# Optimization experiments

Hardware: AMD Instinct MI355X
Metric: run time of the kernel (lower is better)

The kernel has to match this reference:

```python
import jax, jax.numpy as jnp
import numpy as np

B, S_ENC, S_DEC, ENC_H, DEC_H = 8, 2048, 2048, 512, 512


def setup_inputs() -> dict:
    key = jax.random.key(0)
    k1, k2, k3 = jax.random.split(key, 3)
    return {
        "enc_hidden_states": jax.random.normal(k1, (B, S_ENC, ENC_H), dtype=jnp.float32),
        "dec_hidden_states": jax.random.normal(k2, (B, S_DEC, DEC_H), dtype=jnp.float32),
        "W_att": jax.random.normal(k3, (ENC_H, DEC_H), dtype=jnp.float32),
    }


def reference(enc_hidden_states, dec_hidden_states, W_att):
    # Project encoder states: [B, S_enc, dec_h]
    enc_proj = jnp.einsum("bse,ed->bsd", enc_hidden_states, W_att)
    # Luong 'general' scores for all decoder timesteps at once: [B, S_dec, S_enc]
    # (original code loops over decoder timesteps via tf.map_fn; this is the
    # equivalent single batched matmul)
    att_logits = jnp.einsum("btd,bsd->bts", dec_hidden_states, enc_proj)
    att_softmax = jax.nn.softmax(att_logits, axis=-1)
    # Attention context vectors: [B, S_dec, enc_h]
    att_vector = jnp.einsum("bts,bse->bte", att_softmax, enc_hidden_states)
    return att_vector
```

## Files before the change

kernel.cpp:

```cpp
#include <hip/hip_runtime.h>
#include <cstdint>


#define DEVINL __device__ __forceinline__

typedef __attribute__((ext_vector_type(8))) short short8;
typedef __attribute__((ext_vector_type(4))) float f32x4;

DEVINL short f2bf(float x) {
    union { float f; uint32_t u; } v; v.f = x;
    uint32_t r = v.u + 0x7FFFu + ((v.u >> 16) & 1u);
    return (short)(r >> 16);
}
DEVINL float bf2f(short h) {
    union { uint32_t u; float f; } v; v.u = ((uint32_t)(uint16_t)h) << 16;
    return v.f;
}

DEVINL void gload_lds16(const void* g, void* l) {
    __builtin_amdgcn_global_load_lds(
        (const __attribute__((address_space(1))) char*)g,
        (__attribute__((address_space(3))) char*)l, 16, 0, 0);
}

__global__ __launch_bounds__(256)
void split_kernel(const float* __restrict__ x, short* __restrict__ hi,
                  short* __restrict__ lo)
{
    long i = ((long)blockIdx.x * 256 + threadIdx.x) * 8;
    f32x4 a = *(const f32x4*)(x + i);
    f32x4 b = *(const f32x4*)(x + i + 4);
    short8 h, l;
#pragma unroll
    for (int j = 0; j < 4; j++) {
        short ha = f2bf(a[j]); h[j] = ha;     l[j] = f2bf(a[j] - bf2f(ha));
        short hb = f2bf(b[j]); h[4 + j] = hb; l[4 + j] = f2bf(b[j] - bf2f(hb));
    }
    *(short8*)(hi + i) = h;
    *(short8*)(lo + i) = l;
}

__global__ __launch_bounds__(256)
void split_w_kernel(const float* __restrict__ w, short* __restrict__ wth,
                    short* __restrict__ wtl)
{
    int idx = blockIdx.x * 256 + threadIdx.x;
    int k = idx >> 9, n = idx & 511;
    float v = w[idx];
    short h = f2bf(v);
    wth[(long)n * 512 + k] = h;
    wtl[(long)n * 512 + k] = f2bf(v - bf2f(h));
}

__global__ __launch_bounds__(256)
void transpose_bf16_kernel(const float* __restrict__ x, short* __restrict__ xt)
{
    __shared__ short tile[32][33];
    const int b  = blockIdx.z;
    const int s0 = blockIdx.x * 32;
    const int e0 = blockIdx.y * 32;
    const float* px = x + (long)b * 2048 * 512;
    short* pt = xt + (long)b * 512 * 2048;
    const int tx = threadIdx.x & 31;
    const int ty = threadIdx.x >> 5;
#pragma unroll
    for (int r = 0; r < 32; r += 8)
        tile[ty + r][tx] = f2bf(px[(long)(s0 + ty + r) * 512 + e0 + tx]);
    __syncthreads();
#pragma unroll
    for (int r = 0; r < 32; r += 8)
        pt[(long)(e0 + ty + r) * 2048 + s0 + tx] = tile[tx][ty + r];
}

template<int NTERMS, bool SPLIT_OUT>
__global__ __launch_bounds__(256, 2)
void gemm_bt(const short* __restrict__ Ah, const short* __restrict__ Al,
             const short* __restrict__ Bh, const short* __restrict__ Bl,
             float* __restrict__ C, short* __restrict__ Ch, short* __restrict__ Cl,
             int K, int lda, int ldb, int ldc,
             long sA, long sB, long sC)
{
    extern __shared__ char smem_raw[];
    constexpr int OPS = (NTERMS == 3) ? 4 : 2;
    constexpr int SET = 128 * 32 * OPS;
    short* smem = (short*)smem_raw;

    const int tid  = threadIdx.x;
    const int wave = tid >> 6;
    const int lane = tid & 63;
    const int quad = lane >> 4;
    const int l16  = lane & 15;
    const int wm   = (wave >> 1) * 64;
    const int wn   = (wave & 1) * 64;

    const long tile_m = (long)blockIdx.y * 128;
    const long tile_n = (long)blockIdx.x * 128;
    const int  bz     = blockIdx.z;

    const short* pAh = Ah + (long)bz * sA;
    const short* pBh = Bh + (long)bz * sB;
    const short* pAl = (NTERMS == 3) ? (Al + (long)bz * sA) : nullptr;
    const short* pBl = (NTERMS == 3) ? (Bl + (long)bz * sB) : nullptr;

    const int srow = tid >> 2;
    const int skq  = (tid & 3) * 8;
    const int lds_off = srow * 32 + skq;
    const long ga0 = (tile_m + srow) * (long)lda + skq;
    const long gb0 = (tile_n + srow) * (long)ldb + skq;

    auto stage = [&](int k0, int buf) {
        short* s   = smem + buf * SET;
        short* ash = s;
        short* bsh = s + 128 * 32;
        gload_lds16(pAh + ga0 + k0,             ash + lds_off);
        gload_lds16(pAh + ga0 + 64l * lda + k0, ash + lds_off + 64 * 32);
        gload_lds16(pBh + gb0 + k0,             bsh + lds_off);
        gload_lds16(pBh + gb0 + 64l * ldb + k0, bsh + lds_off + 64 * 32);
        if constexpr (NTERMS == 3) {
            short* asl = s + 2 * 128 * 32;
            short* bsl = s + 3 * 128 * 32;
            gload_lds16(pAl + ga0 + k0,             asl + lds_off);
            gload_lds16(pAl + ga0 + 64l * lda + k0, asl + lds_off + 64 * 32);
            gload_lds16(pBl + gb0 + k0,             bsl + lds_off);
            gload_lds16(pBl + gb0 + 64l * ldb + k0, bsl + lds_off + 64 * 32);
        }
    };

    f32x4 acc[4][4] = {};
    stage(0, 0);
    int cur = 0;

    for (int k0 = 0; k0 < K; k0 += 32) {
        __syncthreads();
        if (k0 + 32 < K) stage(k0 + 32, cur ^ 1);

        short* s   = smem + cur * SET;
        short* ash = s;
        short* bsh = s + 128 * 32;
        short* asl = s + 2 * 128 * 32;
        short* bsl = s + 3 * 128 * 32;

        short8 ah[4], bh[4], al[4], bl[4];
#pragma unroll
        for (int i = 0; i < 4; i++) {
            ah[i] = *(const short8*)&ash[(wm + i * 16 + l16) * 32 + quad * 8];
            bh[i] = *(const short8*)&bsh[(wn + i * 16 + l16) * 32 + quad * 8];
            if constexpr (NTERMS == 3) {
                al[i] = *(const short8*)&asl[(wm + i * 16 + l16) * 32 + quad * 8];
                bl[i] = *(const short8*)&bsl[(wn + i * 16 + l16) * 32 + quad * 8];
            }
        }
#pragma unroll
        for (int i = 0; i < 4; i++)
#pragma unroll
            for (int j = 0; j < 4; j++) {
                acc[i][j] = __builtin_amdgcn_mfma_f32_16x16x32_bf16(ah[i], bh[j], acc[i][j], 0, 0, 0);
                if constexpr (NTERMS == 3) {
                    acc[i][j] = __builtin_amdgcn_mfma_f32_16x16x32_bf16(ah[i], bl[j], acc[i][j], 0, 0, 0);
                    acc[i][j] = __builtin_amdgcn_mfma_f32_16x16x32_bf16(al[i], bh[j], acc[i][j], 0, 0, 0);
                }
            }
        cur ^= 1;
    }

#pragma unroll
    for (int i = 0; i < 4; i++)
#pragma unroll
        for (int j = 0; j < 4; j++) {
            const long row0 = tile_m + wm + i * 16 + quad * 4;
            const long col  = tile_n + wn + j * 16 + l16;
#pragma unroll
            for (int r = 0; r < 4; r++) {
                float v = acc[i][j][r];
                if constexpr (SPLIT_OUT) {
                    long idx = (long)bz * sC + (row0 + r) * (long)ldc + col;
                    short h = f2bf(v);
                    Ch[idx] = h;
                    Cl[idx] = f2bf(v - bf2f(h));
                } else {
                    C[(long)bz * sC + (row0 + r) * (long)ldc + col] = v;
                }
            }
        }
}

__global__ __launch_bounds__(256)
void softmax_kernel(const float* __restrict__ logits, short* __restrict__ P)
{
    const long row = blockIdx.x;
    const float* p = logits + row * 2048;
    const int tid = threadIdx.x;
    const int lane = tid & 63, wave = tid >> 6;

    f32x4 v0 = *(const f32x4*)(p + tid * 8);
    f32x4 v1 = *(const f32x4*)(p + tid * 8 + 4);

    float m = fmaxf(fmaxf(fmaxf(v0[0], v0[1]), fmaxf(v0[2], v0[3])),
                    fmaxf(fmaxf(v1[0], v1[1]), fmaxf(v1[2], v1[3])));
#pragma unroll
    for (int o = 32; o > 0; o >>= 1) m = fmaxf(m, __shfl_xor(m, o));

    __shared__ float red[8];
    if (lane == 0) red[wave] = m;
    __syncthreads();
    m = fmaxf(fmaxf(red[0], red[1]), fmaxf(red[2], red[3]));

    float e[8];
    float s = 0.f;
#pragma unroll
    for (int i = 0; i < 4; i++) { e[i] = __expf(v0[i] - m); s += e[i]; }
#pragma unroll
    for (int i = 0; i < 4; i++) { e[4 + i] = __expf(v1[i] - m); s += e[4 + i]; }
#pragma unroll
    for (int o = 32; o > 0; o >>= 1) s += __shfl_xor(s, o);
    if (lane == 0) red[4 + wave] = s;
    __syncthreads();
    const float inv = 1.f / (red[4] + red[5] + red[6] + red[7]);

    short8 ob;
#pragma unroll
    for (int i = 0; i < 8; i++) ob[i] = f2bf(e[i] * inv);
    *(short8*)(P + row * 2048 + tid * 8) = ob;
}

extern "C" void kernel_launch(void* const* d_in, const int* in_sizes, int n_in,
                              void* d_out, int out_size, void* d_ws, size_t ws_size,
                              hipStream_t stream)
{
    const float* enc = (const float*)d_in[0];
    const float* dec = (const float*)d_in[1];
    const float* W   = (const float*)d_in[2];
    float* out = (float*)d_out;

    const long BSE = 8l * 2048 * 512;
    const long NW  = 512l * 512;

    char* p = (char*)d_ws;
    auto take = [&](long bytes) { char* r = p; p += (bytes + 255) & ~255l; return r; };
    short* enc_hi = (short*)take(BSE * 2);
    short* enc_lo = (short*)take(BSE * 2);
    short* dec_hi = (short*)take(BSE * 2);
    short* dec_lo = (short*)take(BSE * 2);
    short* ep_hi  = (short*)take(BSE * 2);
    short* ep_lo  = (short*)take(BSE * 2);
    short* enc_t  = (short*)take(BSE * 2);
    short* wt_hi  = (short*)take(NW * 2);
    short* wt_lo  = (short*)take(NW * 2);
    float* logits = (float*)take(8l * 2048 * 2048 * 4);
    short* Pbuf = enc_hi;
    (void)ws_size; (void)in_sizes; (void)n_in; (void)out_size;

    split_kernel<<<4096, 256, 0, stream>>>(enc, enc_hi, enc_lo);
    split_kernel<<<4096, 256, 0, stream>>>(dec, dec_hi, dec_lo);
    split_w_kernel<<<1024, 256, 0, stream>>>(W, wt_hi, wt_lo);
    transpose_bf16_kernel<<<dim3(64, 16, 8), 256, 0, stream>>>(enc, enc_t);

    gemm_bt<3, true><<<dim3(4, 128, 1), 256, 64 * 1024, stream>>>(
        enc_hi, enc_lo, wt_hi, wt_lo, nullptr, ep_hi, ep_lo,
        512, 512, 512, 512, 0, 0, 0);

    gemm_bt<3, false><<<dim3(16, 16, 8), 256, 64 * 1024, stream>>>(
        dec_hi, dec_lo, ep_hi, ep_lo, logits, nullptr, nullptr,
        512, 512, 512, 2048, 2048l * 512, 2048l * 512, 2048l * 2048);

    softmax_kernel<<<16384, 256, 0, stream>>>(logits, Pbuf);

    gemm_bt<1, false><<<dim3(4, 16, 8), 256, 32 * 1024, stream>>>(
        Pbuf, nullptr, enc_t, nullptr, out, nullptr, nullptr,
        2048, 2048, 2048, 512, 2048l * 2048, 512l * 2048, 2048l * 512);
}
```

Measured before the change: 355.8 us.

## Fuse softmax into logits GEMM epilogue stats and PV GEMM prologue

The logits GEMM epilogue now computes per-tile row max and exp-sum partials. A small combine kernel merges them into a row max and inverse sum. The P·V GEMM reads fp32 logits directly, applies exp(x - m) while staging its A operand into LDS, and scales by the inverse sum at output. This removes the standalone softmax pass and the bf16 P buffer round trip, and the transpose now reads the existing bf16 hi split instead of fp32. The cost is that the PV kernel reads fp32 logits (twice the bytes of bf16 P) and does the exp inline, and the logits GEMM needs extra LDS and reduction syncs.

```diff
diff --git a/kernel.cpp b/kernel.cpp
--- a/kernel.cpp
+++ b/kernel.cpp
@@ -53,30 +53,31 @@
 }
 
 __global__ __launch_bounds__(256)
-void transpose_bf16_kernel(const float* __restrict__ x, short* __restrict__ xt)
+void transpose_bf16_kernel(const short* __restrict__ x, short* __restrict__ xt)
 {
     __shared__ short tile[32][33];
     const int b  = blockIdx.z;
     const int s0 = blockIdx.x * 32;
     const int e0 = blockIdx.y * 32;
-    const float* px = x + (long)b * 2048 * 512;
+    const short* px = x + (long)b * 2048 * 512;
     short* pt = xt + (long)b * 512 * 2048;
     const int tx = threadIdx.x & 31;
     const int ty = threadIdx.x >> 5;
 #pragma unroll
     for (int r = 0; r < 32; r += 8)
-        tile[ty + r][tx] = f2bf(px[(long)(s0 + ty + r) * 512 + e0 + tx]);
+        tile[ty + r][tx] = px[(long)(s0 + ty + r) * 512 + e0 + tx];
     __syncthreads();
 #pragma unroll
     for (int r = 0; r < 32; r += 8)
         pt[(long)(e0 + ty + r) * 2048 + s0 + tx] = tile[tx][ty + r];
 }
 
-template<int NTERMS, bool SPLIT_OUT>
+template<int NTERMS, bool SPLIT_OUT, bool STATS>
 __global__ __launch_bounds__(256, 2)
 void gemm_bt(const short* __restrict__ Ah, const short* __restrict__ Al,
              const short* __restrict__ Bh, const short* __restrict__ Bl,
              float* __restrict__ C, short* __restrict__ Ch, short* __restrict__ Cl,
+             float2* __restrict__ stats,
              int K, int lda, int ldb, int ldc,
              long sA, long sB, long sC)
 {
@@ -163,6 +164,74 @@
         cur ^= 1;
     }
 
+    if constexpr (STATS) {
+        float* sred = (float*)(smem + 2 * SET);
+        float mrow[4][4], lrow[4][4];
+#pragma unroll
+        for (int i = 0; i < 4; i++)
+#pragma unroll
+            for (int r = 0; r < 4; r++) {
+                float m = acc[i][0][r];
+#pragma unroll
+                for (int j = 1; j < 4; j++) m = fmaxf(m, acc[i][j][r]);
+                m = fmaxf(m, __shfl_xor(m, 1));
+                m = fmaxf(m, __shfl_xor(m, 2));
+                m = fmaxf(m, __shfl_xor(m, 4));
+                m = fmaxf(m, __shfl_xor(m, 8));
+                mrow[i][r] = m;
+            }
+        __syncthreads();
+        if (l16 == 0) {
+#pragma unroll
+            for (int i = 0; i < 4; i++)
+#pragma unroll
+                for (int r = 0; r < 4; r++)
+                    sred[(wm + i * 16 + quad * 4 + r) * 2 + (wave & 1)] = mrow[i][r];
+        }
+        __syncthreads();
+#pragma unroll
+        for (int i = 0; i < 4; i++)
+#pragma unroll
+            for (int r = 0; r < 4; r++) {
+                int row = wm + i * 16 + quad * 4 + r;
+                mrow[i][r] = fmaxf(sred[row * 2], sred[row * 2 + 1]);
+            }
+        __syncthreads();
+#pragma unroll
+        for (int i = 0; i < 4; i++)
+#pragma unroll
+            for (int r = 0; r < 4; r++) {
+                float s = 0.f;
+#pragma unroll
+                for (int j = 0; j < 4; j++) s += __expf(acc[i][j][r] - mrow[i][r]);
+                s += __shfl_xor(s, 1);
+                s += __shfl_xor(s, 2);
+                s += __shfl_xor(s, 4);
+                s += __shfl_xor(s, 8);
+                lrow[i][r] = s;
+            }
+        if (l16 == 0) {
+#pragma unroll
+            for (int i = 0; i < 4; i++)
+#pragma unroll
+                for (int r = 0; r < 4; r++)
+                    sred[(wm + i * 16 + quad * 4 + r) * 2 + (wave & 1)] = lrow[i][r];
+        }
+        __syncthreads();
+        if ((wave & 1) == 0 && l16 == 0) {
+#pragma unroll
+            for (int i = 0; i < 4; i++)
+#pragma unroll
+                for (int r = 0; r < 4; r++) {
+                    int row = wm + i * 16 + quad * 4 + r;
+                    long grow = tile_m + row;
+                    float2 v; v.x = mrow[i][r];
+                    v.y = sred[row * 2] + sred[row * 2 + 1];
+                    stats[((long)bz * 2048 + grow) * 16 + blockIdx.x] = v;
+                }
+        }
+    }
+
 #pragma unroll
     for (int i = 0; i < 4; i++)
 #pragma unroll
@@ -185,42 +254,126 @@
 }
 
 __global__ __launch_bounds__(256)
-void softmax_kernel(const float* __restrict__ logits, short* __restrict__ P)
-{
-    const long row = blockIdx.x;
-    const float* p = logits + row * 2048;
-    const int tid = threadIdx.x;
-    const int lane = tid & 63, wave = tid >> 6;
-
-    f32x4 v0 = *(const f32x4*)(p + tid * 8);
-    f32x4 v1 = *(const f32x4*)(p + tid * 8 + 4);
-
-    float m = fmaxf(fmaxf(fmaxf(v0[0], v0[1]), fmaxf(v0[2], v0[3])),
-                    fmaxf(fmaxf(v1[0], v1[1]), fmaxf(v1[2], v1[3])));
-#pragma unroll
-    for (int o = 32; o > 0; o >>= 1) m = fmaxf(m, __shfl_xor(m, o));
-
-    __shared__ float red[8];
-    if (lane == 0) red[wave] = m;
-    __syncthreads();
-    m = fmaxf(fmaxf(red[0], red[1]), fmaxf(red[2], red[3]));
-
-    float e[8];
-    float s = 0.f;
-#pragma unroll
-    for (int i = 0; i < 4; i++) { e[i] = __expf(v0[i] - m); s += e[i]; }
-#pragma unroll
-    for (int i = 0; i < 4; i++) { e[4 + i] = __expf(v1[i] - m); s += e[4 + i]; }
-#pragma unroll
-    for (int o = 32; o > 0; o >>= 1) s += __shfl_xor(s, o);
-    if (lane == 0) red[4 + wave] = s;
-    __syncthreads();
-    const float inv = 1.f / (red[4] + red[5] + red[6] + red[7]);
-
-    short8 ob;
-#pragma unroll
-    for (int i = 0; i < 8; i++) ob[i] = f2bf(e[i] * inv);
-    *(short8*)(P + row * 2048 + tid * 8) = ob;
+void combine_kernel(const float2* __restrict__ stats, float* __restrict__ Mrow,
+                    float* __restrict__ Linv)
+{
+    long r = (long)blockIdx.x * 256 + threadIdx.x;
+    const float2* s = stats + r * 16;
+    float2 v[16];
+#pragma unroll
+    for (int i = 0; i < 16; i++) v[i] = s[i];
+    float m = v[0].x;
+#pragma unroll
+    for (int i = 1; i < 16; i++) m = fmaxf(m, v[i].x);
+    float l = 0.f;
+#pragma unroll
+    for (int i = 0; i < 16; i++) l += v[i].y * __expf(v[i].x - m);
+    Mrow[r] = m;
+    Linv[r] = 1.f / l;
+}
+
+__global__ __launch_bounds__(256, 2)
+void pv_fused(const float* __restrict__ S, const short* __restrict__ encT,
+              const float* __restrict__ Mrow, const float* __restrict__ Linv,
+              float* __restrict__ Out)
+{
+    extern __shared__ char smem_raw[];
+    short* smem = (short*)smem_raw;
+    constexpr int ABUF = 128 * 32;
+
+    const int tid  = threadIdx.x;
+    const int wave = tid >> 6;
+    const int lane = tid & 63;
+    const int quad = lane >> 4;
+    const int l16  = lane & 15;
+    const int wm   = (wave >> 1) * 64;
+    const int wn   = (wave & 1) * 64;
+
+    const int  bz     = blockIdx.z;
+    const long tile_m = (long)blockIdx.y * 128;
+    const long tile_n = (long)blockIdx.x * 128;
+
+    const int arow = tid >> 1;
+    const int ascol = (tid & 1) * 16;
+    const float* pS = S + ((long)bz * 2048 + tile_m + arow) * 2048 + ascol;
+    const int aw_off = arow * 32 + ascol;
+    const float m_r = Mrow[bz * 2048 + tile_m + arow];
+
+    const short* pB = encT + (long)bz * 512 * 2048 + (tile_n + (tid >> 2)) * 2048 + (tid & 3) * 8;
+    const int b_lds = (tid >> 2) * 32 + (tid & 3) * 8;
+
+    f32x4 acc[4][4] = {};
+    float a_pre[16];
+
+#pragma unroll
+    for (int c = 0; c < 4; c++) *(f32x4*)&a_pre[c * 4] = *(const f32x4*)(pS + c * 4);
+    gload_lds16(pB,             smem + 2 * ABUF + b_lds);
+    gload_lds16(pB + 64 * 2048, smem + 2 * ABUF + b_lds + 64 * 32);
+    {
+        short8 h0, h1;
+#pragma unroll
+        for (int e = 0; e < 8; e++) h0[e] = f2bf(__expf(a_pre[e] - m_r));
+#pragma unroll
+        for (int e = 0; e < 8; e++) h1[e] = f2bf(__expf(a_pre[8 + e] - m_r));
+        *(short8*)(smem + aw_off)     = h0;
+        *(short8*)(smem + aw_off + 8) = h1;
+    }
+    int cur = 0;
+
+    for (int k0 = 0; k0 < 2048; k0 += 32) {
+        __syncthreads();
+        const bool more = (k0 + 32 < 2048);
+        if (more) {
+            const float* ps = pS + k0 + 32;
+#pragma unroll
+            for (int c = 0; c < 4; c++) *(f32x4*)&a_pre[c * 4] = *(const f32x4*)(ps + c * 4);
+            gload_lds16(pB + k0 + 32,             smem + (2 + (cur ^ 1)) * ABUF + b_lds);
+            gload_lds16(pB + 64 * 2048 + k0 + 32, smem + (2 + (cur ^ 1)) * ABUF + b_lds + 64 * 32);
+        }
+
+        short* Ac = smem + cur * ABUF;
+        short* Bc = smem + (2 + cur) * ABUF;
+        short8 a[4], b[4];
+#pragma unroll
+        for (int i = 0; i < 4; i++) {
+            a[i] = *(const short8*)&Ac[(wm + i * 16 + l16) * 32 + quad * 8];
+            b[i] = *(const short8*)&Bc[(wn + i * 16 + l16) * 32 + quad * 8];
+        }
+#pragma unroll
+        for (int i = 0; i < 4; i++)
+#pragma unroll
+            for (int j = 0; j < 4; j++)
+                acc[i][j] = __builtin_amdgcn_mfma_f32_16x16x32_bf16(a[i], b[j], acc[i][j], 0, 0, 0);
+
+        if (more) {
+            short8 h0, h1;
+#pragma unroll
+            for (int e = 0; e < 8; e++) h0[e] = f2bf(__expf(a_pre[e] - m_r));
+#pragma unroll
+            for (int e = 0; e < 8; e++) h1[e] = f2bf(__expf(a_pre[8 + e] - m_r));
+            short* An = smem + (cur ^ 1) * ABUF;
+            *(short8*)(An + aw_off)     = h0;
+            *(short8*)(An + aw_off + 8) = h1;
+        }
+        cur ^= 1;
+    }
+
+    float li[4][4];
+#pragma unroll
+    for (int i = 0; i < 4; i++)
+#pragma unroll
+        for (int r = 0; r < 4; r++)
+            li[i][r] = Linv[bz * 2048 + tile_m + wm + i * 16 + quad * 4 + r];
+#pragma unroll
+    for (int i = 0; i < 4; i++)
+#pragma unroll
+        for (int j = 0; j < 4; j++) {
+            const long row0 = tile_m + wm + i * 16 + quad * 4;
+            const long col  = tile_n + wn + j * 16 + l16;
+#pragma unroll
+            for (int r = 0; r < 4; r++)
+                Out[((long)bz * 2048 + row0 + r) * 512 + col] = acc[i][j][r] * li[i][r];
+        }
 }
 
 extern "C" void kernel_launch(void* const* d_in, const int* in_sizes, int n_in,
@@ -247,25 +400,26 @@
     short* wt_hi  = (short*)take(NW * 2);
     short* wt_lo  = (short*)take(NW * 2);
     float* logits = (float*)take(8l * 2048 * 2048 * 4);
-    short* Pbuf = enc_hi;
+    float2* stats = (float2*)enc_lo;
+    float*  MrowA = (float*)(enc_lo + 4l * 1024 * 1024);
+    float*  LinvA = (float*)(enc_lo + 5l * 1024 * 1024);
     (void)ws_size; (void)in_sizes; (void)n_in; (void)out_size;
 
     split_kernel<<<4096, 256, 0, stream>>>(enc, enc_hi, enc_lo);
     split_kernel<<<4096, 256, 0, stream>>>(dec, dec_hi, dec_lo);
     split_w_kernel<<<1024, 256, 0, stream>>>(W, wt_hi, wt_lo);
-    transpose_bf16_kernel<<<dim3(64, 16, 8), 256, 0, stream>>>(enc, enc_t);
-
-    gemm_bt<3, true><<<dim3(4, 128, 1), 256, 64 * 1024, stream>>>(
-        enc_hi, enc_lo, wt_hi, wt_lo, nullptr, ep_hi, ep_lo,
+    transpose_bf16_kernel<<<dim3(64, 16, 8), 256, 0, stream>>>(enc_hi, enc_t);
+
+    gemm_bt<3, true, false><<<dim3(4, 128, 1), 256, 64 * 1024, stream>>>(
+        enc_hi, enc_lo, wt_hi, wt_lo, nullptr, ep_hi, ep_lo, nullptr,
         512, 512, 512, 512, 0, 0, 0);
 
-    gemm_bt<3, false><<<dim3(16, 16, 8), 256, 64 * 1024, stream>>>(
-        dec_hi, dec_lo, ep_hi, ep_lo, logits, nullptr, nullptr,
+    gemm_bt<3, false, true><<<dim3(16, 16, 8), 256, 64 * 1024 + 1024, stream>>>(
+        dec_hi, dec_lo, ep_hi, ep_lo, logits, nullptr, nullptr, stats,
         512, 512, 512, 2048, 2048l * 512, 2048l * 512, 2048l * 2048);
 
-    softmax_kernel<<<16384, 256, 0, stream>>>(logits, Pbuf);
-
-    gemm_bt<1, false><<<dim3(4, 16, 8), 256, 32 * 1024, stream>>>(
-        Pbuf, nullptr, enc_t, nullptr, out, nullptr, nullptr,
-        2048, 2048, 2048, 512, 2048l * 2048, 512l * 2048, 2048l * 512);
-}
+    combine_kernel<<<64, 256, 0, stream>>>(stats, MrowA, LinvA);
+
+    pv_fused<<<dim3(4, 16, 8), 256, 32 * 1024, stream>>>(
+        logits, enc_t, MrowA, LinvA, out);
+}
```

Measured after the change: 419.8 us. 18.0% more time.
